# Performance work log

Measured on AMD Instinct MI355X. Metric: run time of the kernel, lower is better.

## Reference

```python
import jax, jax.numpy as jnp
import numpy as np
from jax import lax

B, L, H, V, INNER = 16, 2048, 512, 32000, 8
LR = 0.01
EPS = 1e-5
STD = 0.02


def setup_inputs() -> dict:
    key = jax.random.key(0)
    ks = jax.random.split(key, 14)
    n = lambda k, shape: (jax.random.normal(k, shape, dtype=jnp.float32) * STD)
    return {
        'seq': jax.random.randint(ks[0], (B, L), 0, V, dtype=jnp.int64),
        'embed': n(ks[1], (V, H)),
        'enc_w1': n(ks[2], (2 * H, H)), 'enc_b1': jnp.zeros((2 * H,), jnp.float32),
        'enc_w2': n(ks[3], (H, 2 * H)), 'enc_b2': jnp.zeros((H,), jnp.float32),
        'ln_w': jnp.ones((H,), jnp.float32), 'ln_b': jnp.zeros((H,), jnp.float32),
        'mlp_w1': n(ks[4], (INNER, H)), 'mlp_b1': jnp.zeros((INNER,), jnp.float32),
        'mlp_w2': n(ks[5], (H, INNER)), 'mlp_b2': jnp.zeros((H,), jnp.float32),
        'out_w': n(ks[6], (V, H)), 'out_b': jnp.zeros((V,), jnp.float32),
    }


def _encoder(seq, embed, enc_w1, enc_b1, enc_w2, enc_b2, ln_w, ln_b):
    h = embed[seq]                                        # [B,L,H]
    ff = jax.nn.relu(h @ enc_w1.T + enc_b1) @ enc_w2.T + enc_b2
    x = h + ff
    mu = jnp.mean(x, axis=-1, keepdims=True)
    var = jnp.mean(jnp.square(x - mu), axis=-1, keepdims=True)  # biased, as torch LayerNorm
    return (x - mu) * lax.rsqrt(var + EPS) * ln_w + ln_b


def _inner_mlp(w1, b1, w2, b2, x):
    return w2 @ jax.nn.relu(w1 @ x + b1) + b2


def _ttt_contexts(hidden, mlp_w1, mlp_b1, mlp_w2, mlp_b2):
    # torch detaches hidden and copies base_mlp weights: no grads flow here
    hidden = lax.stop_gradient(hidden)
    p0 = tuple(lax.stop_gradient(p) for p in (mlp_w1, mlp_b1, mlp_w2, mlp_b2))
    ts = np.arange(0, L - 3, 2)                           # 1023 sequential steps
    keys = hidden[:, ts]                                  # [B,T,H]
    vals = hidden[:, ts + 1]                              # [B,T,H]
    query = hidden[:, -1]                                 # [B,H]

    def step(p, kv):
        w1, b1, w2, b2 = p
        k, v = kv
        def loss(w1, b1, w2, b2):
            pred = _inner_mlp(w1, b1, w2, b2, k)
            return jnp.mean(jnp.square(pred - v))
        g1, gb1, g2, gb2 = jax.grad(loss, argnums=(0, 1, 2, 3))(w1, b1, w2, b2)
        return (w1 - LR * g1, b1 - LR * gb1, w2 - LR * g2, b2 - LR * gb2), None

    def run(kb, vb, qb):
        (w1, b1, w2, b2), _ = lax.scan(step, p0, (kb, vb))
        return _inner_mlp(w1, b1, w2, b2, qb)

    return jax.vmap(run)(keys, vals, query)               # [B,H]


def reference(seq, embed, enc_w1, enc_b1, enc_w2, enc_b2, ln_w, ln_b,
              mlp_w1, mlp_b1, mlp_w2, mlp_b2, out_w, out_b):
    hidden = _encoder(seq, embed, enc_w1, enc_b1, enc_w2, enc_b2, ln_w, ln_b)
    ctx = _ttt_contexts(hidden, mlp_w1, mlp_b1, mlp_w2, mlp_b2)
    return ctx @ out_w.T + out_b                          # [B,V]
```

## Files before the change

kernel.cpp:

```cpp
#include <hip/hip_runtime.h>

#define GAS __attribute__((address_space(1)))
#define LAS __attribute__((address_space(3)))

typedef __attribute__((ext_vector_type(8))) short bf16x8;
typedef __attribute__((ext_vector_type(4))) float f32x4;
typedef __attribute__((ext_vector_type(2))) float f32x2;

static constexpr int Bb = 16, Ll = 2048, Hh = 512, Vv = 32000, H2 = 1024;
static constexpr int Mtot = Bb * Ll;
static constexpr float LRc = 0.01f, EPSc = 1e-5f;

static constexpr size_t OFF_X    = 0;
static constexpr size_t OFF_EBF  = OFF_X   + (size_t)Mtot * Hh * 4;
static constexpr size_t OFF_W1BF = OFF_EBF + (size_t)Vv * Hh * 2;
static constexpr size_t OFF_W2BF = OFF_W1BF + (size_t)H2 * Hh * 2;
static constexpr size_t OFF_CTX  = OFF_W2BF + (size_t)Hh * H2 * 2;
static constexpr size_t OFF_FF1  = OFF_CTX + (size_t)Bb * Hh * 4;

__device__ inline unsigned short f2bf(float f) {
  unsigned u = __float_as_uint(f);
  return (unsigned short)((u + 0x7fffu + ((u >> 16) & 1u)) >> 16);
}

__device__ inline f32x2 pk_fma(f32x2 a, f32x2 b, f32x2 c) { return a * b + c; }

#define DPP_ADD(ctrl)                                                        \
  {                                                                          \
    int t_ = __builtin_amdgcn_update_dpp(0, v_, ctrl, 0xf, 0xf, true);       \
    v_ = __float_as_int(__int_as_float(v_) + __int_as_float(t_));            \
  }
__device__ inline float wsum_bcast(float x) {
  int v_ = __float_as_int(x);
  DPP_ADD(0x111)
  DPP_ADD(0x112)
  DPP_ADD(0x114)
  DPP_ADD(0x118)
  DPP_ADD(0x142)
  DPP_ADD(0x143)
  return __int_as_float(__builtin_amdgcn_readlane(v_, 63));
}

__global__ __launch_bounds__(256) void cvt_bf16_kernel(const float* __restrict__ src,
                                                       unsigned short* __restrict__ dst, int n8) {
  int stride = gridDim.x * blockDim.x;
  for (int i = blockIdx.x * blockDim.x + threadIdx.x; i < n8; i += stride) {
    const float4* p = (const float4*)(src + (size_t)i * 8);
    float4 a = p[0], b = p[1];
    uint4 o;
    o.x = f2bf(a.x) | ((unsigned)f2bf(a.y) << 16);
    o.y = f2bf(a.z) | ((unsigned)f2bf(a.w) << 16);
    o.z = f2bf(b.x) | ((unsigned)f2bf(b.y) << 16);
    o.w = f2bf(b.z) | ((unsigned)f2bf(b.w) << 16);
    *(uint4*)(dst + (size_t)i * 8) = o;
  }
}

template <int KTOT, bool GATHER, bool RELUOUT>
__global__ __launch_bounds__(256) void gemm_bt(const unsigned short* __restrict__ Abase,
                                               const int* __restrict__ seq, int seq_off,
                                               const unsigned short* __restrict__ Bmat,
                                               const float* __restrict__ bias,
                                               unsigned short* __restrict__ outb,
                                               float* __restrict__ outf,
                                               int out_row_off, int ldout) {
  __shared__ unsigned short As[128 * 32];
  __shared__ unsigned short Bs[128 * 32];
  __shared__ unsigned long long aoff[128];
  const int tid = threadIdx.x;
  const int m0 = blockIdx.x * 128, n0 = blockIdx.y * 128;

  if (tid < 128) {
    long long r;
    if (GATHER) r = (long long)seq[seq_off + m0 + tid] * KTOT;
    else        r = (long long)(m0 + tid) * KTOT;
    aoff[tid] = (unsigned long long)r;
  }
  __syncthreads();

  const int srow = tid >> 2;
  const int scol = (tid & 3) * 8;
  const int wave = tid >> 6;
  const int lane = tid & 63;
  const int wr = wave >> 1, wc = wave & 1;
  const int fr = lane & 15;
  const int fk = (lane >> 4) * 8;

  f32x4 acc[4][4] = {};

  for (int k0 = 0; k0 < KTOT; k0 += 32) {
#pragma unroll
    for (int i = 0; i < 2; ++i) {
      const unsigned short* ga = Abase + aoff[i * 64 + srow] + k0 + scol;
      __builtin_amdgcn_global_load_lds((const GAS void*)ga,
          (LAS void*)((char*)As + i * 4096 + wave * 1024), 16, 0, 0);
      const unsigned short* gb = Bmat + (size_t)(n0 + i * 64 + srow) * KTOT + k0 + scol;
      __builtin_amdgcn_global_load_lds((const GAS void*)gb,
          (LAS void*)((char*)Bs + i * 4096 + wave * 1024), 16, 0, 0);
    }
    __syncthreads();
    bf16x8 af[4], bfr[4];
#pragma unroll
    for (int m = 0; m < 4; ++m)
      af[m] = *(const bf16x8*)&As[(wr * 64 + m * 16 + fr) * 32 + fk];
#pragma unroll
    for (int n = 0; n < 4; ++n)
      bfr[n] = *(const bf16x8*)&Bs[(wc * 64 + n * 16 + fr) * 32 + fk];
#pragma unroll
    for (int m = 0; m < 4; ++m)
#pragma unroll
      for (int n = 0; n < 4; ++n)
        acc[m][n] = __builtin_amdgcn_mfma_f32_16x16x32_bf16(af[m], bfr[n], acc[m][n], 0, 0, 0);
    __syncthreads();
  }

  float bv[4];
#pragma unroll
  for (int n = 0; n < 4; ++n) bv[n] = bias[n0 + wc * 64 + n * 16 + fr];
#pragma unroll
  for (int m = 0; m < 4; ++m) {
#pragma unroll
    for (int n = 0; n < 4; ++n) {
#pragma unroll
      for (int j = 0; j < 4; ++j) {
        int rl = wr * 64 + m * 16 + ((lane >> 4) << 2) + j;
        int col = n0 + wc * 64 + n * 16 + fr;
        float v = acc[m][n][j] + bv[n];
        size_t off = (size_t)(out_row_off + m0 + rl) * ldout + col;
        if (RELUOUT) { v = fmaxf(v, 0.f); outb[off] = f2bf(v); }
        else outf[off] = v;
      }
    }
  }
}

__global__ __launch_bounds__(256) void ln_kernel(float* __restrict__ xbuf,
                                                 const float* __restrict__ embed,
                                                 const int* __restrict__ seq,
                                                 const float* __restrict__ lnw,
                                                 const float* __restrict__ lnb) {
  int row = blockIdx.x * 4 + (threadIdx.x >> 6);
  int lane = threadIdx.x & 63;
  int c = lane * 8;
  int s = seq[row];
  float* xr = xbuf + (size_t)row * Hh;
  const float* hr = embed + (size_t)s * Hh;
  float4 f0 = *(const float4*)(xr + c), f1 = *(const float4*)(xr + c + 4);
  float4 h0 = *(const float4*)(hr + c), h1 = *(const float4*)(hr + c + 4);
  float x[8] = {f0.x + h0.x, f0.y + h0.y, f0.z + h0.z, f0.w + h0.w,
                f1.x + h1.x, f1.y + h1.y, f1.z + h1.z, f1.w + h1.w};
  float sm = 0.f, sq = 0.f;
#pragma unroll
  for (int u = 0; u < 8; ++u) { sm += x[u]; sq += x[u] * x[u]; }
#pragma unroll
  for (int m = 1; m < 64; m <<= 1) { sm += __shfl_xor(sm, m, 64); sq += __shfl_xor(sq, m, 64); }
  float mu = sm * (1.f / 512.f);
  float var = sq * (1.f / 512.f) - mu * mu;
  float rs = rsqrtf(var + EPSc);
  float y[8];
#pragma unroll
  for (int u = 0; u < 8; ++u) y[u] = (x[u] - mu) * rs * lnw[c + u] + lnb[c + u];
  *(float4*)(xr + c) = make_float4(y[0], y[1], y[2], y[3]);
  *(float4*)(xr + c + 4) = make_float4(y[4], y[5], y[6], y[7]);
}

__global__ __launch_bounds__(64, 1) void ttt_kernel(const float* __restrict__ hidden,
                                                    const float* __restrict__ w1_0,
                                                    const float* __restrict__ b1_0,
                                                    const float* __restrict__ w2_0,
                                                    const float* __restrict__ b2_0,
                                                    float* __restrict__ ctx) {
  const int b = blockIdx.x;
  const int l = threadIdx.x;
  const int c0 = l * 8;
  const float* hb = hidden + (size_t)b * Ll * Hh;
  const float scale = 2.0f / 512.0f;

  f32x2 W1v[8][4];
  f32x2 W2v[8][4];
  float B1u[8];
  float B2[8];
#pragma unroll
  for (int j = 0; j < 8; ++j) {
    float4 a = *(const float4*)(w1_0 + (size_t)j * Hh + c0);
    float4 d = *(const float4*)(w1_0 + (size_t)j * Hh + c0 + 4);
    W1v[j][0] = f32x2{a.x, a.y}; W1v[j][1] = f32x2{a.z, a.w};
    W1v[j][2] = f32x2{d.x, d.y}; W1v[j][3] = f32x2{d.z, d.w};
    B1u[j] = b1_0[j];
  }
#pragma unroll
  for (int u = 0; u < 8; ++u) {
    float4 a = *(const float4*)(w2_0 + (size_t)(c0 + u) * 8);
    float4 d = *(const float4*)(w2_0 + (size_t)(c0 + u) * 8 + 4);
    W2v[u][0] = f32x2{a.x, a.y}; W2v[u][1] = f32x2{a.z, a.w};
    W2v[u][2] = f32x2{d.x, d.y}; W2v[u][3] = f32x2{d.z, d.w};
  }
  {
    float4 e = *(const float4*)(b2_0 + c0);
    float4 f = *(const float4*)(b2_0 + c0 + 4);
    B2[0] = e.x; B2[1] = e.y; B2[2] = e.z; B2[3] = e.w;
    B2[4] = f.x; B2[5] = f.y; B2[6] = f.z; B2[7] = f.w;
  }

  f32x2 Kc[4], Kn[4];
  float Vs[8];
  {
    const float* p0 = hb + c0;
    float4 a = *(const float4*)p0, d = *(const float4*)(p0 + 4);
    Kc[0] = f32x2{a.x, a.y}; Kc[1] = f32x2{a.z, a.w};
    Kc[2] = f32x2{d.x, d.y}; Kc[3] = f32x2{d.z, d.w};
    const float* p1 = hb + 2 * Hh + c0;
    float4 e = *(const float4*)p1, f = *(const float4*)(p1 + 4);
    Kn[0] = f32x2{e.x, e.y}; Kn[1] = f32x2{e.z, e.w};
    Kn[2] = f32x2{f.x, f.y}; Kn[3] = f32x2{f.z, f.w};
    const float* pv = hb + Hh + c0;
    float4 g = *(const float4*)pv, h4 = *(const float4*)(pv + 4);
    Vs[0] = g.x; Vs[1] = g.y; Vs[2] = g.z; Vs[3] = g.w;
    Vs[4] = h4.x; Vs[5] = h4.y; Vs[6] = h4.z; Vs[7] = h4.w;
  }

  float zu[8];
#pragma unroll
  for (int j = 0; j < 8; ++j) {
    f32x2 acc = {0.f, 0.f};
#pragma unroll
    for (int p = 0; p < 4; ++p) acc = pk_fma(W1v[j][p], Kc[p], acc);
    zu[j] = wsum_bcast(acc.x + acc.y) + B1u[j];
  }

#pragma unroll 3
  for (int t = 0; t < 1023; ++t) {
    float4 ka, kb, va, vb;
    {
      const float* pf = hb + (size_t)(2 * t + 4) * Hh + c0;
      ka = *(const float4*)pf; kb = *(const float4*)(pf + 4);
      const float* pv = hb + (size_t)(2 * t + 3) * Hh + c0;
      va = *(const float4*)pv; vb = *(const float4*)(pv + 4);
    }

    float kap;
    {
      f32x2 acc = {0.f, 0.f};
#pragma unroll
      for (int p = 0; p < 4; ++p) acc = pk_fma(Kc[p], Kn[p], acc);
      kap = wsum_bcast(acc.x + acc.y);
    }
    float ys[8];
#pragma unroll
    for (int j = 0; j < 8; ++j) {
      f32x2 acc = {0.f, 0.f};
#pragma unroll
      for (int p = 0; p < 4; ++p) acc = pk_fma(W1v[j][p], Kn[p], acc);
      ys[j] = wsum_bcast(acc.x + acc.y);
    }

    float hu[8];
#pragma unroll
    for (int j = 0; j < 8; ++j) hu[j] = fmaxf(zu[j], 0.f);
    f32x2 h2[4];
#pragma unroll
    for (int p = 0; p < 4; ++p) h2[p] = f32x2{hu[2 * p], hu[2 * p + 1]};
    const f32x2 nlr = {-LRc, -LRc};
    f32x2 nh2[4];
#pragma unroll
    for (int p = 0; p < 4; ++p) nh2[p] = h2[p] * nlr;

    float d_[8];
    f32x2 dd[8];
#pragma unroll
    for (int u = 0; u < 8; ++u) {
      f32x2 acc = {0.f, 0.f};
#pragma unroll
      for (int p = 0; p < 4; ++p) acc = pk_fma(W2v[u][p], h2[p], acc);
      float pred = acc.x + acc.y + B2[u];
      float dv = (pred - Vs[u]) * scale;
      d_[u] = dv;
      dd[u] = f32x2{dv, dv};
    }

    f32x2 dhp[4] = {{0.f, 0.f}, {0.f, 0.f}, {0.f, 0.f}, {0.f, 0.f}};
#pragma unroll
    for (int u = 0; u < 8; ++u)
#pragma unroll
      for (int p = 0; p < 4; ++p) dhp[p] = pk_fma(W2v[u][p], dd[u], dhp[p]);

    float dz[8];
#pragma unroll
    for (int p = 0; p < 4; ++p) {
      float s0 = wsum_bcast(dhp[p].x);
      float s1 = wsum_bcast(dhp[p].y);
      dz[2 * p]     = (zu[2 * p]     > 0.f) ? s0 : 0.f;
      dz[2 * p + 1] = (zu[2 * p + 1] > 0.f) ? s1 : 0.f;
    }

    float t1 = -LRc * (kap + 1.f);
#pragma unroll
    for (int j = 0; j < 8; ++j) zu[j] = (ys[j] + B1u[j]) + t1 * dz[j];

#pragma unroll
    for (int u = 0; u < 8; ++u) {
#pragma unroll
      for (int p = 0; p < 4; ++p) W2v[u][p] = pk_fma(dd[u], nh2[p], W2v[u][p]);
      B2[u] = fmaf(-LRc, d_[u], B2[u]);
    }
#pragma unroll
    for (int j = 0; j < 8; ++j) {
      float g = -LRc * dz[j];
      f32x2 gv = {g, g};
#pragma unroll
      for (int p = 0; p < 4; ++p) W1v[j][p] = pk_fma(gv, Kc[p], W1v[j][p]);
      B1u[j] = fmaf(-LRc, dz[j], B1u[j]);
    }

#pragma unroll
    for (int p = 0; p < 4; ++p) Kc[p] = Kn[p];
    Kn[0] = f32x2{ka.x, ka.y}; Kn[1] = f32x2{ka.z, ka.w};
    Kn[2] = f32x2{kb.x, kb.y}; Kn[3] = f32x2{kb.z, kb.w};
    Vs[0] = va.x; Vs[1] = va.y; Vs[2] = va.z; Vs[3] = va.w;
    Vs[4] = vb.x; Vs[5] = vb.y; Vs[6] = vb.z; Vs[7] = vb.w;
  }

  {
    const float* pq = hb + (size_t)(Ll - 1) * Hh + c0;
    float4 a = *(const float4*)pq, d = *(const float4*)(pq + 4);
    f32x2 Q[4] = {f32x2{a.x, a.y}, f32x2{a.z, a.w}, f32x2{d.x, d.y}, f32x2{d.z, d.w}};
    float hq[8];
#pragma unroll
    for (int j = 0; j < 8; ++j) {
      f32x2 acc = {0.f, 0.f};
#pragma unroll
      for (int p = 0; p < 4; ++p) acc = pk_fma(W1v[j][p], Q[p], acc);
      hq[j] = fmaxf(wsum_bcast(acc.x + acc.y) + B1u[j], 0.f);
    }
    f32x2 h2[4];
#pragma unroll
    for (int p = 0; p < 4; ++p) h2[p] = f32x2{hq[2 * p], hq[2 * p + 1]};
    float o[8];
#pragma unroll
    for (int u = 0; u < 8; ++u) {
      f32x2 acc = {0.f, 0.f};
#pragma unroll
      for (int p = 0; p < 4; ++p) acc = pk_fma(W2v[u][p], h2[p], acc);
      o[u] = acc.x + acc.y + B2[u];
    }
    float* cp = ctx + (size_t)b * Hh + c0;
    *(float4*)cp = make_float4(o[0], o[1], o[2], o[3]);
    *(float4*)(cp + 4) = make_float4(o[4], o[5], o[6], o[7]);
  }
}

__global__ __launch_bounds__(256) void out_kernel(const float* __restrict__ ctx,
                                                  const float* __restrict__ outw,
                                                  const float* __restrict__ outb_,
                                                  float* __restrict__ out) {
  __shared__ float cs[16 * 516];
  int tid = threadIdx.x;
#pragma unroll
  for (int r = 0; r < 32; ++r) {
    int idx = r * 256 + tid;
    cs[(idx >> 9) * 516 + (idx & 511)] = ctx[idx];
  }
  __syncthreads();
  int v = blockIdx.x * 16 + (tid >> 4);
  int b = tid & 15;
  const float4* wr = (const float4*)(outw + (size_t)v * 512);
  const float4* cr = (const float4*)(cs + b * 516);
  float acc = 0.f;
#pragma unroll 8
  for (int k = 0; k < 128; ++k) {
    float4 wv = wr[k];
    float4 cv = cr[k];
    acc += wv.x * cv.x + wv.y * cv.y + wv.z * cv.z + wv.w * cv.w;
  }
  out[(size_t)b * 32000 + v] = acc + outb_[v];
}

extern "C" void kernel_launch(void* const* d_in, const int* in_sizes, int n_in,
                              void* d_out, int out_size, void* d_ws, size_t ws_size,
                              hipStream_t stream) {
  const int*   seq    = (const int*)d_in[0];
  const float* embed  = (const float*)d_in[1];
  const float* enc_w1 = (const float*)d_in[2];
  const float* enc_b1 = (const float*)d_in[3];
  const float* enc_w2 = (const float*)d_in[4];
  const float* enc_b2 = (const float*)d_in[5];
  const float* ln_w   = (const float*)d_in[6];
  const float* ln_b   = (const float*)d_in[7];
  const float* mlp_w1 = (const float*)d_in[8];
  const float* mlp_b1 = (const float*)d_in[9];
  const float* mlp_w2 = (const float*)d_in[10];
  const float* mlp_b2 = (const float*)d_in[11];
  const float* out_w  = (const float*)d_in[12];
  const float* out_b  = (const float*)d_in[13];
  float* out = (float*)d_out;

  char* ws = (char*)d_ws;
  float*          xbuf = (float*)(ws + OFF_X);
  unsigned short* ebf  = (unsigned short*)(ws + OFF_EBF);
  unsigned short* w1bf = (unsigned short*)(ws + OFF_W1BF);
  unsigned short* w2bf = (unsigned short*)(ws + OFF_W2BF);
  float*          ctx  = (float*)(ws + OFF_CTX);
  unsigned short* ff1  = (unsigned short*)(ws + OFF_FF1);

  const int cand[4] = {1, 2, 4, 8};
  int nc = 8;
  for (int ci = 0; ci < 4; ++ci) {
    if (OFF_FF1 + (size_t)(Mtot / cand[ci]) * H2 * 2 <= ws_size) { nc = cand[ci]; break; }
  }

  cvt_bf16_kernel<<<2048, 256, 0, stream>>>(embed, ebf, Vv * Hh / 8);
  cvt_bf16_kernel<<<256, 256, 0, stream>>>(enc_w1, w1bf, H2 * Hh / 8);
  cvt_bf16_kernel<<<256, 256, 0, stream>>>(enc_w2, w2bf, Hh * H2 / 8);

  const int Mc = Mtot / nc;
  for (int c = 0; c < nc; ++c) {
    const int m0 = c * Mc;
    gemm_bt<512, true, true><<<dim3(Mc / 128, 8), 256, 0, stream>>>(
        ebf, seq, m0, w1bf, enc_b1, ff1, nullptr, 0, H2);
    gemm_bt<1024, false, false><<<dim3(Mc / 128, 4), 256, 0, stream>>>(
        ff1, nullptr, 0, w2bf, enc_b2, nullptr, xbuf, m0, Hh);
  }
  ln_kernel<<<Mtot / 4, 256, 0, stream>>>(xbuf, embed, seq, ln_w, ln_b);
  ttt_kernel<<<Bb, 64, 0, stream>>>(xbuf, mlp_w1, mlp_b1, mlp_w2, mlp_b2, ctx);
  out_kernel<<<Vv / 16, 256, 0, stream>>>(ctx, out_w, out_b, out);
}
```

Before: 1.078 ms.

## Restructure TTT step to defer W1 update and batch all wave reductions

Reworks the sequential TTT loop so the W1/b1 gradient update from the previous step is applied lazily at the start of the next step. This lets the dh, W1·k_next and k·k_next reductions for a step be done together in one batched butterfly of 17 values using shfl_xor, replacing 17 separate serial DPP-plus-readlane reductions. The learning-rate and loss scale are folded into one constant, and the FMA loops are reordered to interleave independent accumulators for ILP. The cost is an extra K register set and more live registers in a 64-thread, single-wave-per-block kernel, and the ds_swizzle/permute based shuffles may be slower than DPP per step.

```diff
diff --git a/kernel.cpp b/kernel.cpp
--- a/kernel.cpp
+++ b/kernel.cpp
@@ -24,22 +24,6 @@
 }
 
 __device__ inline f32x2 pk_fma(f32x2 a, f32x2 b, f32x2 c) { return a * b + c; }
-
-#define DPP_ADD(ctrl)                                                        \
-  {                                                                          \
-    int t_ = __builtin_amdgcn_update_dpp(0, v_, ctrl, 0xf, 0xf, true);       \
-    v_ = __float_as_int(__int_as_float(v_) + __int_as_float(t_));            \
-  }
-__device__ inline float wsum_bcast(float x) {
-  int v_ = __float_as_int(x);
-  DPP_ADD(0x111)
-  DPP_ADD(0x112)
-  DPP_ADD(0x114)
-  DPP_ADD(0x118)
-  DPP_ADD(0x142)
-  DPP_ADD(0x143)
-  return __int_as_float(__builtin_amdgcn_readlane(v_, 63));
-}
 
 __global__ __launch_bounds__(256) void cvt_bf16_kernel(const float* __restrict__ src,
                                                        unsigned short* __restrict__ dst, int n8) {
@@ -174,7 +158,7 @@
   const int l = threadIdx.x;
   const int c0 = l * 8;
   const float* hb = hidden + (size_t)b * Ll * Hh;
-  const float scale = 2.0f / 512.0f;
+  const float cs = -LRc * 2.0f / 512.0f;
 
   f32x2 W1v[8][4];
   f32x2 W2v[8][4];
@@ -202,7 +186,7 @@
     B2[4] = f.x; B2[5] = f.y; B2[6] = f.z; B2[7] = f.w;
   }
 
-  f32x2 Kc[4], Kn[4];
+  f32x2 Kp[4], Kc[4], Kn[4];
   float Vs[8];
   {
     const float* p0 = hb + c0;
@@ -213,69 +197,77 @@
     float4 e = *(const float4*)p1, f = *(const float4*)(p1 + 4);
     Kn[0] = f32x2{e.x, e.y}; Kn[1] = f32x2{e.z, e.w};
     Kn[2] = f32x2{f.x, f.y}; Kn[3] = f32x2{f.z, f.w};
+#pragma unroll
+    for (int p = 0; p < 4; ++p) Kp[p] = Kc[p];
     const float* pv = hb + Hh + c0;
     float4 g = *(const float4*)pv, h4 = *(const float4*)(pv + 4);
     Vs[0] = g.x; Vs[1] = g.y; Vs[2] = g.z; Vs[3] = g.w;
     Vs[4] = h4.x; Vs[5] = h4.y; Vs[6] = h4.z; Vs[7] = h4.w;
   }
 
-  float zu[8];
-#pragma unroll
-  for (int j = 0; j < 8; ++j) {
-    f32x2 acc = {0.f, 0.f};
-#pragma unroll
-    for (int p = 0; p < 4; ++p) acc = pk_fma(W1v[j][p], Kc[p], acc);
-    zu[j] = wsum_bcast(acc.x + acc.y) + B1u[j];
-  }
-
-#pragma unroll 3
+  float ST[8], dhLT[8], kapT, zu[8];
+  {
+    f32x2 acc[8] = {};
+#pragma unroll
+    for (int p = 0; p < 4; ++p)
+#pragma unroll
+      for (int j = 0; j < 8; ++j) acc[j] = pk_fma(W1v[j][p], Kc[p], acc[j]);
+    float ch[8];
+#pragma unroll
+    for (int j = 0; j < 8; ++j) ch[j] = acc[j].x + acc[j].y;
+#pragma unroll
+    for (int st = 0; st < 6; ++st) {
+      float tmp[8];
+#pragma unroll
+      for (int c = 0; c < 8; ++c) tmp[c] = __shfl_xor(ch[c], 1 << st, 64);
+#pragma unroll
+      for (int c = 0; c < 8; ++c) ch[c] += tmp[c];
+    }
+#pragma unroll
+    for (int j = 0; j < 8; ++j) { ST[j] = ch[j]; dhLT[j] = 0.f; zu[j] = -1.f; }
+    kapT = 0.f;
+  }
+
+#pragma unroll 2
   for (int t = 0; t < 1023; ++t) {
-    float4 ka, kb, va, vb;
-    {
-      const float* pf = hb + (size_t)(2 * t + 4) * Hh + c0;
-      ka = *(const float4*)pf; kb = *(const float4*)(pf + 4);
-      const float* pv = hb + (size_t)(2 * t + 3) * Hh + c0;
-      va = *(const float4*)pv; vb = *(const float4*)(pv + 4);
-    }
-
-    float kap;
-    {
-      f32x2 acc = {0.f, 0.f};
-#pragma unroll
-      for (int p = 0; p < 4; ++p) acc = pk_fma(Kc[p], Kn[p], acc);
-      kap = wsum_bcast(acc.x + acc.y);
-    }
-    float ys[8];
-#pragma unroll
-    for (int j = 0; j < 8; ++j) {
-      f32x2 acc = {0.f, 0.f};
-#pragma unroll
-      for (int p = 0; p < 4; ++p) acc = pk_fma(W1v[j][p], Kn[p], acc);
-      ys[j] = wsum_bcast(acc.x + acc.y);
-    }
-
-    float hu[8];
-#pragma unroll
-    for (int j = 0; j < 8; ++j) hu[j] = fmaxf(zu[j], 0.f);
+    const float* kr = hb + (size_t)(2 * t + 4) * Hh + c0;
+    float4 ka = *(const float4*)kr, kb4 = *(const float4*)(kr + 4);
+    const float* vr = hb + (size_t)(2 * t + 3) * Hh + c0;
+    float4 va = *(const float4*)vr, vb = *(const float4*)(vr + 4);
+
+    float dzL[8], z[8];
+    float kap1 = kapT + 1.f;
+#pragma unroll
+    for (int j = 0; j < 8; ++j) dzL[j] = (zu[j] > 0.f) ? dhLT[j] : 0.f;
+#pragma unroll
+    for (int j = 0; j < 8; ++j) z[j] = fmaf(dzL[j], kap1, ST[j] + B1u[j]);
+#pragma unroll
+    for (int j = 0; j < 8; ++j) B1u[j] += dzL[j];
+#pragma unroll
+    for (int p = 0; p < 4; ++p)
+#pragma unroll
+      for (int j = 0; j < 8; ++j)
+        W1v[j][p] = pk_fma(f32x2{dzL[j], dzL[j]}, Kp[p], W1v[j][p]);
+
+    float h[8];
+#pragma unroll
+    for (int j = 0; j < 8; ++j) h[j] = fmaxf(z[j], 0.f);
     f32x2 h2[4];
 #pragma unroll
-    for (int p = 0; p < 4; ++p) h2[p] = f32x2{hu[2 * p], hu[2 * p + 1]};
-    const f32x2 nlr = {-LRc, -LRc};
-    f32x2 nh2[4];
-#pragma unroll
-    for (int p = 0; p < 4; ++p) nh2[p] = h2[p] * nlr;
-
-    float d_[8];
+    for (int p = 0; p < 4; ++p) h2[p] = f32x2{h[2 * p], h[2 * p + 1]};
+
+    f32x2 pac[8] = {};
+#pragma unroll
+    for (int p = 0; p < 4; ++p)
+#pragma unroll
+      for (int u = 0; u < 8; ++u) pac[u] = pk_fma(W2v[u][p], h2[p], pac[u]);
+    float dL[8];
     f32x2 dd[8];
 #pragma unroll
     for (int u = 0; u < 8; ++u) {
-      f32x2 acc = {0.f, 0.f};
-#pragma unroll
-      for (int p = 0; p < 4; ++p) acc = pk_fma(W2v[u][p], h2[p], acc);
-      float pred = acc.x + acc.y + B2[u];
-      float dv = (pred - Vs[u]) * scale;
-      d_[u] = dv;
-      dd[u] = f32x2{dv, dv};
+      float pred = pac[u].x + pac[u].y + B2[u];
+      dL[u] = (pred - Vs[u]) * cs;
+      dd[u] = f32x2{dL[u], dL[u]};
     }
 
     f32x2 dhp[4] = {{0.f, 0.f}, {0.f, 0.f}, {0.f, 0.f}, {0.f, 0.f}};
@@ -284,65 +276,94 @@
 #pragma unroll
       for (int p = 0; p < 4; ++p) dhp[p] = pk_fma(W2v[u][p], dd[u], dhp[p]);
 
-    float dz[8];
-#pragma unroll
-    for (int p = 0; p < 4; ++p) {
-      float s0 = wsum_bcast(dhp[p].x);
-      float s1 = wsum_bcast(dhp[p].y);
-      dz[2 * p]     = (zu[2 * p]     > 0.f) ? s0 : 0.f;
-      dz[2 * p + 1] = (zu[2 * p + 1] > 0.f) ? s1 : 0.f;
-    }
-
-    float t1 = -LRc * (kap + 1.f);
-#pragma unroll
-    for (int j = 0; j < 8; ++j) zu[j] = (ys[j] + B1u[j]) + t1 * dz[j];
-
-#pragma unroll
-    for (int u = 0; u < 8; ++u) {
-#pragma unroll
-      for (int p = 0; p < 4; ++p) W2v[u][p] = pk_fma(dd[u], nh2[p], W2v[u][p]);
-      B2[u] = fmaf(-LRc, d_[u], B2[u]);
-    }
-#pragma unroll
-    for (int j = 0; j < 8; ++j) {
-      float g = -LRc * dz[j];
-      f32x2 gv = {g, g};
-#pragma unroll
-      for (int p = 0; p < 4; ++p) W1v[j][p] = pk_fma(gv, Kc[p], W1v[j][p]);
-      B1u[j] = fmaf(-LRc, dz[j], B1u[j]);
-    }
-
-#pragma unroll
-    for (int p = 0; p < 4; ++p) Kc[p] = Kn[p];
+    f32x2 sac[8] = {};
+#pragma unroll
+    for (int p = 0; p < 4; ++p)
+#pragma unroll
+      for (int j = 0; j < 8; ++j) sac[j] = pk_fma(W1v[j][p], Kn[p], sac[j]);
+    f32x2 kac = {0.f, 0.f};
+#pragma unroll
+    for (int p = 0; p < 4; ++p) kac = pk_fma(Kc[p], Kn[p], kac);
+
+    float ch[17];
+#pragma unroll
+    for (int p = 0; p < 4; ++p) { ch[2 * p] = dhp[p].x; ch[2 * p + 1] = dhp[p].y; }
+#pragma unroll
+    for (int j = 0; j < 8; ++j) ch[8 + j] = sac[j].x + sac[j].y;
+    ch[16] = kac.x + kac.y;
+
+#pragma unroll
+    for (int st = 0; st < 6; ++st) {
+      float tmp[17];
+#pragma unroll
+      for (int c = 0; c < 17; ++c) tmp[c] = __shfl_xor(ch[c], 1 << st, 64);
+#pragma unroll
+      for (int c = 0; c < 17; ++c) ch[c] += tmp[c];
+    }
+
+#pragma unroll
+    for (int p = 0; p < 4; ++p)
+#pragma unroll
+      for (int u = 0; u < 8; ++u) W2v[u][p] = pk_fma(dd[u], h2[p], W2v[u][p]);
+#pragma unroll
+    for (int u = 0; u < 8; ++u) B2[u] += dL[u];
+
+#pragma unroll
+    for (int j = 0; j < 8; ++j) { dhLT[j] = ch[j]; ST[j] = ch[8 + j]; zu[j] = z[j]; }
+    kapT = ch[16];
+#pragma unroll
+    for (int p = 0; p < 4; ++p) { Kp[p] = Kc[p]; Kc[p] = Kn[p]; }
     Kn[0] = f32x2{ka.x, ka.y}; Kn[1] = f32x2{ka.z, ka.w};
-    Kn[2] = f32x2{kb.x, kb.y}; Kn[3] = f32x2{kb.z, kb.w};
+    Kn[2] = f32x2{kb4.x, kb4.y}; Kn[3] = f32x2{kb4.z, kb4.w};
     Vs[0] = va.x; Vs[1] = va.y; Vs[2] = va.z; Vs[3] = va.w;
     Vs[4] = vb.x; Vs[5] = vb.y; Vs[6] = vb.z; Vs[7] = vb.w;
   }
 
   {
+    float dzL[8];
+#pragma unroll
+    for (int j = 0; j < 8; ++j) dzL[j] = (zu[j] > 0.f) ? dhLT[j] : 0.f;
+#pragma unroll
+    for (int j = 0; j < 8; ++j) B1u[j] += dzL[j];
+#pragma unroll
+    for (int p = 0; p < 4; ++p)
+#pragma unroll
+      for (int j = 0; j < 8; ++j)
+        W1v[j][p] = pk_fma(f32x2{dzL[j], dzL[j]}, Kp[p], W1v[j][p]);
+
     const float* pq = hb + (size_t)(Ll - 1) * Hh + c0;
     float4 a = *(const float4*)pq, d = *(const float4*)(pq + 4);
     f32x2 Q[4] = {f32x2{a.x, a.y}, f32x2{a.z, a.w}, f32x2{d.x, d.y}, f32x2{d.z, d.w}};
+    f32x2 qac[8] = {};
+#pragma unroll
+    for (int p = 0; p < 4; ++p)
+#pragma unroll
+      for (int j = 0; j < 8; ++j) qac[j] = pk_fma(W1v[j][p], Q[p], qac[j]);
+    float ch[8];
+#pragma unroll
+    for (int j = 0; j < 8; ++j) ch[j] = qac[j].x + qac[j].y;
+#pragma unroll
+    for (int st = 0; st < 6; ++st) {
+      float tmp[8];
+#pragma unroll
+      for (int c = 0; c < 8; ++c) tmp[c] = __shfl_xor(ch[c], 1 << st, 64);
+#pragma unroll
+      for (int c = 0; c < 8; ++c) ch[c] += tmp[c];
+    }
     float hq[8];
 #pragma unroll
-    for (int j = 0; j < 8; ++j) {
-      f32x2 acc = {0.f, 0.f};
-#pragma unroll
-      for (int p = 0; p < 4; ++p) acc = pk_fma(W1v[j][p], Q[p], acc);
-      hq[j] = fmaxf(wsum_bcast(acc.x + acc.y) + B1u[j], 0.f);
-    }
-    f32x2 h2[4];
-#pragma unroll
-    for (int p = 0; p < 4; ++p) h2[p] = f32x2{hq[2 * p], hq[2 * p + 1]};
+    for (int j = 0; j < 8; ++j) hq[j] = fmaxf(ch[j] + B1u[j], 0.f);
+    f32x2 hq2[4];
+#pragma unroll
+    for (int p = 0; p < 4; ++p) hq2[p] = f32x2{hq[2 * p], hq[2 * p + 1]};
+    f32x2 oac[8] = {};
+#pragma unroll
+    for (int p = 0; p < 4; ++p)
+#pragma unroll
+      for (int u = 0; u < 8; ++u) oac[u] = pk_fma(W2v[u][p], hq2[p], oac[u]);
     float o[8];
 #pragma unroll
-    for (int u = 0; u < 8; ++u) {
-      f32x2 acc = {0.f, 0.f};
-#pragma unroll
-      for (int p = 0; p < 4; ++p) acc = pk_fma(W2v[u][p], h2[p], acc);
-      o[u] = acc.x + acc.y + B2[u];
-    }
+    for (int u = 0; u < 8; ++u) o[u] = oac[u].x + oac[u].y + B2[u];
     float* cp = ctx + (size_t)b * Hh + c0;
     *(float4*)cp = make_float4(o[0], o[1], o[2], o[3]);
     *(float4*)(cp + 4) = make_float4(o[4], o[5], o[6], o[7]);
```

After: 1.466 ms. +36.0%, slower.
